# Kernel tuning notes

Measured on AMD Instinct MI355X. Metric: run time of the kernel, lower is better.

The kernel has to match this reference:

```python
import jax, jax.numpy as jnp
import numpy as np

NUM_HEADS = 16

def setup_inputs() -> dict:
    key = jax.random.key(0)
    k1, k2, k3 = jax.random.split(key, 3)
    D = 1024
    return {
        "hidden_states": jax.random.normal(k1, (2, 2048, D), dtype=jnp.float32),
        "c_attn_w": jax.random.normal(k2, (D, 3 * D), dtype=jnp.float32) * 0.02,
        "c_attn_b": jnp.zeros((3 * D,), dtype=jnp.float32),
        "c_proj_w": jax.random.normal(k3, (D, D), dtype=jnp.float32) * 0.02,
        "c_proj_b": jnp.zeros((D,), dtype=jnp.float32),
    }

def reference(hidden_states, c_attn_w, c_attn_b, c_proj_w, c_proj_b):
    B, S, D = hidden_states.shape
    H = NUM_HEADS
    hd = D // H
    # Conv1D: x @ W + b, then split into q, k, v
    qkv = hidden_states @ c_attn_w + c_attn_b  # [B, S, 3D]
    q, k, v = jnp.split(qkv, 3, axis=-1)
    q = q.reshape(B, S, H, hd).transpose(0, 2, 1, 3)  # [B, H, S, hd]
    k = k.reshape(B, S, H, hd).transpose(0, 2, 1, 3)
    v = v.reshape(B, S, H, hd).transpose(0, 2, 1, 3)
    # scaled QK^T
    scores = jnp.einsum("bhqd,bhkd->bhqk", q, k) / jnp.asarray(hd ** 0.5, q.dtype)
    # causal mask (tril), masked positions set to dtype min per original code
    causal = jnp.tril(jnp.ones((S, S), dtype=bool))
    mask_value = jnp.finfo(scores.dtype).min
    scores = jnp.where(causal[None, None], scores, mask_value)
    attn = jax.nn.softmax(scores, axis=-1)
    out = jnp.einsum("bhqk,bhkd->bhqd", attn, v)  # [B, H, S, hd]
    out = out.transpose(0, 2, 1, 3).reshape(B, S, D)
    out = out @ c_proj_w + c_proj_b
    return out
```

## Files before the change

kernel.cpp:

```cpp
#include <hip/hip_runtime.h>
#include <hip/hip_bf16.h>
#include <math.h>

#define B_ 2
#define S_ 2048
#define D_ 1024
#define H_ 16
#define HD 64
#define M_ (B_ * S_)
#define N_QKV (3 * D_)

typedef short short8 __attribute__((ext_vector_type(8)));
typedef float floatx4 __attribute__((ext_vector_type(4)));

static __device__ __forceinline__ unsigned short f2bf(float x) {
    __hip_bfloat16 h = __float2bfloat16(x);
    unsigned short u;
    __builtin_memcpy(&u, &h, sizeof(u));
    return u;
}
static __device__ __forceinline__ float bf2f(unsigned short b) {
    union { unsigned u; float f; } v; v.u = ((unsigned)b) << 16;
    return v.f;
}
static __device__ __forceinline__ void split2(float x, unsigned short& h, unsigned short& l) {
    h = f2bf(x);
    l = f2bf(x - bf2f(h));
}

static __device__ __forceinline__ void dma16(const void* g, void* l) {
    __builtin_amdgcn_global_load_lds(
        (const __attribute__((address_space(1))) unsigned int*)g,
        (__attribute__((address_space(3))) unsigned int*)l,
        16, 0, 0);
}

__global__ __launch_bounds__(256) void prep_wT(
    const float* __restrict__ W, int N,
    unsigned short* __restrict__ Thi, unsigned short* __restrict__ Tlo)
{
    __shared__ float Ws[64][68];
    const int t  = threadIdx.x;
    const int n0 = blockIdx.x * 64, k0 = blockIdx.y * 64;
    {
        const int kl = t >> 4, nl = (t & 15) * 4;
        const float* src = W + (size_t)(k0 + kl) * N + n0 + nl;
#pragma unroll
        for (int g = 0; g < 4; g++)
            *(float4*)&Ws[kl + g * 16][nl] = *(const float4*)(src + (size_t)g * 16 * N);
    }
    __syncthreads();
    {
        const int nl = t >> 2, ks = (t & 3) * 16;
        short8 h0, h1, l0, l1;
#pragma unroll
        for (int j = 0; j < 8; j++) {
            unsigned short hh, ll;
            split2(Ws[ks + j][nl], hh, ll);
            h0[j] = (short)hh; l0[j] = (short)ll;
        }
#pragma unroll
        for (int j = 0; j < 8; j++) {
            unsigned short hh, ll;
            split2(Ws[ks + 8 + j][nl], hh, ll);
            h1[j] = (short)hh; l1[j] = (short)ll;
        }
        unsigned short* dh = Thi + (size_t)(n0 + nl) * D_ + k0 + ks;
        unsigned short* dl = Tlo + (size_t)(n0 + nl) * D_ + k0 + ks;
        *(short8*)dh = h0; *(short8*)(dh + 8) = h1;
        *(short8*)dl = l0; *(short8*)(dl + 8) = l1;
    }
}

__global__ __launch_bounds__(256) void gemm_qkv(
    const float* __restrict__ A,
    const unsigned short* __restrict__ BThi, const unsigned short* __restrict__ BTlo,
    const float* __restrict__ bias,
    unsigned short* __restrict__ Qhi, unsigned short* __restrict__ Qlo,
    unsigned short* __restrict__ Khi, unsigned short* __restrict__ Klo,
    unsigned short* __restrict__ vThi, unsigned short* __restrict__ vTlo)
{
    __shared__ unsigned short sAh[128 * 32], sAl[128 * 32];
    __shared__ unsigned short sBh[128 * 32], sBl[128 * 32];

    const int t    = threadIdx.x;
    const int m0   = blockIdx.y * 128, n0 = blockIdx.x * 128;
    const int lane = t & 63, wave = t >> 6;
    const int lm   = lane & 15, quad = lane >> 4;
    const int wm   = (wave >> 1) * 64, wn = (wave & 1) * 64;

    const int srow = t >> 1, sseg = (t & 1) * 16;
    const float* Ap = A + (size_t)(m0 + srow) * D_ + sseg;

    const int lrow = lane >> 2, lcol = (lane & 3) * 8;
    const unsigned short* gBh0 = BThi + (size_t)(n0 + wave * 32 + lrow) * D_ + lcol;
    const unsigned short* gBl0 = BTlo + (size_t)(n0 + wave * 32 + lrow) * D_ + lcol;
    unsigned short* lBh0 = sBh + wave * 1024 + lane * 8;
    unsigned short* lBl0 = sBl + wave * 1024 + lane * 8;

    floatx4 acc[4][4];
#pragma unroll
    for (int i = 0; i < 4; i++)
#pragma unroll
        for (int j = 0; j < 4; j++)
#pragma unroll
            for (int r = 0; r < 4; r++) acc[i][j][r] = 0.f;

    float4 af[4];
    af[0] = *(const float4*)(Ap);     af[1] = *(const float4*)(Ap + 4);
    af[2] = *(const float4*)(Ap + 8); af[3] = *(const float4*)(Ap + 12);

    for (int k0 = 0; k0 < D_; k0 += 32) {
        short8 ah0, ah1, al0, al1;
#pragma unroll
        for (int g = 0; g < 4; g++) {
            float xs[4] = {af[g].x, af[g].y, af[g].z, af[g].w};
#pragma unroll
            for (int e = 0; e < 4; e++) {
                unsigned short hh, ll;
                split2(xs[e], hh, ll);
                if (g < 2) { ah0[g * 4 + e] = (short)hh; al0[g * 4 + e] = (short)ll; }
                else       { ah1[(g - 2) * 4 + e] = (short)hh; al1[(g - 2) * 4 + e] = (short)ll; }
            }
        }
        __syncthreads();
        {
            unsigned short* a = &sAh[srow * 32 + sseg];
            unsigned short* b = &sAl[srow * 32 + sseg];
            *(short8*)a = ah0; *(short8*)(a + 8) = ah1;
            *(short8*)b = al0; *(short8*)(b + 8) = al1;
        }
        dma16(gBh0 + k0, lBh0);
        dma16(gBh0 + (size_t)16 * D_ + k0, lBh0 + 512);
        dma16(gBl0 + k0, lBl0);
        dma16(gBl0 + (size_t)16 * D_ + k0, lBl0 + 512);
        __syncthreads();

        if (k0 + 32 < D_) {
            const float* an = Ap + k0 + 32;
            af[0] = *(const float4*)(an);     af[1] = *(const float4*)(an + 4);
            af[2] = *(const float4*)(an + 8); af[3] = *(const float4*)(an + 12);
        }

        short8 bhf[4], blf[4];
#pragma unroll
        for (int nb = 0; nb < 4; nb++) {
            const int r = wn + nb * 16 + lm;
            bhf[nb] = *(const short8*)&sBh[r * 32 + quad * 8];
            blf[nb] = *(const short8*)&sBl[r * 32 + quad * 8];
        }
#pragma unroll
        for (int mb = 0; mb < 4; mb++) {
            const int r = wm + mb * 16 + lm;
            short8 ah = *(const short8*)&sAh[r * 32 + quad * 8];
            short8 al = *(const short8*)&sAl[r * 32 + quad * 8];
#pragma unroll
            for (int nb = 0; nb < 4; nb++) {
                acc[mb][nb] = __builtin_amdgcn_mfma_f32_16x16x32_bf16(ah, bhf[nb], acc[mb][nb], 0, 0, 0);
                acc[mb][nb] = __builtin_amdgcn_mfma_f32_16x16x32_bf16(al, bhf[nb], acc[mb][nb], 0, 0, 0);
                acc[mb][nb] = __builtin_amdgcn_mfma_f32_16x16x32_bf16(ah, blf[nb], acc[mb][nb], 0, 0, 0);
            }
        }
    }

    const int nmode = n0 >> 10;
    if (nmode == 0) {
#pragma unroll
        for (int nb = 0; nb < 4; nb++) {
            const int c = n0 + wn + nb * 16 + lm;
            const float bv = bias[c];
#pragma unroll
            for (int mb = 0; mb < 4; mb++) {
                const int rowb = m0 + wm + mb * 16 + quad * 4;
#pragma unroll
                for (int r = 0; r < 4; r++) {
                    unsigned short hh, ll;
                    split2((acc[mb][nb][r] + bv) * 0.125f, hh, ll);
                    Qhi[(size_t)(rowb + r) * D_ + c] = hh;
                    Qlo[(size_t)(rowb + r) * D_ + c] = ll;
                }
            }
        }
    } else if (nmode == 1) {
#pragma unroll
        for (int nb = 0; nb < 4; nb++) {
            const int c = n0 + wn + nb * 16 + lm;
            const float bv = bias[c];
            const int cq = c - 1024;
#pragma unroll
            for (int mb = 0; mb < 4; mb++) {
                const int rowb = m0 + wm + mb * 16 + quad * 4;
#pragma unroll
                for (int r = 0; r < 4; r++) {
                    unsigned short hh, ll;
                    split2(acc[mb][nb][r] + bv, hh, ll);
                    Khi[(size_t)(rowb + r) * D_ + cq] = hh;
                    Klo[(size_t)(rowb + r) * D_ + cq] = ll;
                }
            }
        }
    } else {
#pragma unroll
        for (int nb = 0; nb < 4; nb++) {
            const int c = n0 + wn + nb * 16 + lm;
            const float bv = bias[c];
            const int cq = c - 2048;
            const int hh_ = cq >> 6, dd = cq & 63;
#pragma unroll
            for (int mb = 0; mb < 4; mb++) {
                const int rowb = m0 + wm + mb * 16 + quad * 4;
                const int bb = rowb >> 11, ss = rowb & 2047;
                unsigned short hv[4], lv[4];
#pragma unroll
                for (int r = 0; r < 4; r++)
                    split2(acc[mb][nb][r] + bv, hv[r], lv[r]);
                const size_t idx = ((size_t)((bb * 16 + hh_) * 64 + dd)) * S_ + ss;
                *(uint2*)&vThi[idx] = make_uint2((unsigned)hv[0] | ((unsigned)hv[1] << 16),
                                                 (unsigned)hv[2] | ((unsigned)hv[3] << 16));
                *(uint2*)&vTlo[idx] = make_uint2((unsigned)lv[0] | ((unsigned)lv[1] << 16),
                                                 (unsigned)lv[2] | ((unsigned)lv[3] << 16));
            }
        }
    }
}

__global__ __launch_bounds__(256) void gemm_out(
    const unsigned short* __restrict__ Ahi, const unsigned short* __restrict__ Alo,
    const unsigned short* __restrict__ BThi, const unsigned short* __restrict__ BTlo,
    const float* __restrict__ bias, float* __restrict__ C)
{
    __shared__ unsigned short sAh[128 * 32], sAl[128 * 32];
    __shared__ unsigned short sBh[128 * 32], sBl[128 * 32];

    const int t    = threadIdx.x;
    const int m0   = blockIdx.y * 128, n0 = blockIdx.x * 128;
    const int lane = t & 63, wave = t >> 6;
    const int lm   = lane & 15, quad = lane >> 4;
    const int wm   = (wave >> 1) * 64, wn = (wave & 1) * 64;

    const int lrow = lane >> 2, lcol = (lane & 3) * 8;
    const unsigned short* gAh = Ahi + (size_t)(m0 + wave * 32 + lrow) * D_ + lcol;
    const unsigned short* gAl = Alo + (size_t)(m0 + wave * 32 + lrow) * D_ + lcol;
    const unsigned short* gBh = BThi + (size_t)(n0 + wave * 32 + lrow) * D_ + lcol;
    const unsigned short* gBl = BTlo + (size_t)(n0 + wave * 32 + lrow) * D_ + lcol;
    unsigned short* lAh = sAh + wave * 1024 + lane * 8;
    unsigned short* lAl = sAl + wave * 1024 + lane * 8;
    unsigned short* lBh = sBh + wave * 1024 + lane * 8;
    unsigned short* lBl = sBl + wave * 1024 + lane * 8;

    floatx4 acc[4][4];
#pragma unroll
    for (int i = 0; i < 4; i++)
#pragma unroll
        for (int j = 0; j < 4; j++)
#pragma unroll
            for (int r = 0; r < 4; r++) acc[i][j][r] = 0.f;

    for (int k0 = 0; k0 < D_; k0 += 32) {
        __syncthreads();
        dma16(gAh + k0, lAh);
        dma16(gAh + (size_t)16 * D_ + k0, lAh + 512);
        dma16(gAl + k0, lAl);
        dma16(gAl + (size_t)16 * D_ + k0, lAl + 512);
        dma16(gBh + k0, lBh);
        dma16(gBh + (size_t)16 * D_ + k0, lBh + 512);
        dma16(gBl + k0, lBl);
        dma16(gBl + (size_t)16 * D_ + k0, lBl + 512);
        __syncthreads();

        short8 bhf[4], blf[4];
#pragma unroll
        for (int nb = 0; nb < 4; nb++) {
            const int r = wn + nb * 16 + lm;
            bhf[nb] = *(const short8*)&sBh[r * 32 + quad * 8];
            blf[nb] = *(const short8*)&sBl[r * 32 + quad * 8];
        }
#pragma unroll
        for (int mb = 0; mb < 4; mb++) {
            const int r = wm + mb * 16 + lm;
            short8 ah = *(const short8*)&sAh[r * 32 + quad * 8];
            short8 al = *(const short8*)&sAl[r * 32 + quad * 8];
#pragma unroll
            for (int nb = 0; nb < 4; nb++) {
                acc[mb][nb] = __builtin_amdgcn_mfma_f32_16x16x32_bf16(ah, bhf[nb], acc[mb][nb], 0, 0, 0);
                acc[mb][nb] = __builtin_amdgcn_mfma_f32_16x16x32_bf16(al, bhf[nb], acc[mb][nb], 0, 0, 0);
                acc[mb][nb] = __builtin_amdgcn_mfma_f32_16x16x32_bf16(ah, blf[nb], acc[mb][nb], 0, 0, 0);
            }
        }
    }

#pragma unroll
    for (int nb = 0; nb < 4; nb++) {
        const int c = n0 + wn + nb * 16 + lm;
        const float bv = bias[c];
#pragma unroll
        for (int mb = 0; mb < 4; mb++) {
            const int rowb = m0 + wm + mb * 16 + quad * 4;
#pragma unroll
            for (int r = 0; r < 4; r++)
                C[(size_t)(rowb + r) * D_ + c] = acc[mb][nb][r] + bv;
        }
    }
}

#define PST 72

__global__ __launch_bounds__(512, 4) void flash_attn_mfma(
    unsigned short* QAhi, unsigned short* QAlo,
    const unsigned short* __restrict__ Khi, const unsigned short* __restrict__ Klo,
    const unsigned short* __restrict__ vThi, const unsigned short* __restrict__ vTlo)
{
    __shared__ unsigned short KhiS[64 * PST];
    __shared__ unsigned short KloS[64 * PST];
    __shared__ unsigned short VhiS[64 * PST];
    __shared__ unsigned short VloS[64 * PST];
    __shared__ unsigned short PhS[128 * PST];
    __shared__ unsigned short PlS[128 * PST];

    const int t    = threadIdx.x;
    const int pj   = blockIdx.x;
    const int bh   = blockIdx.y;
    const int b    = bh >> 4, h = bh & 15;
    const int lane = t & 63, w = t >> 6;
    const int lm   = lane & 15, quad = lane >> 4;

    const int srow = t >> 3;
    const int sseg = (t & 7) * 8;

    const unsigned short* Kh_b = Khi + (size_t)(b * S_) * D_ + h * HD + sseg;
    const unsigned short* Kl_b = Klo + (size_t)(b * S_) * D_ + h * HD + sseg;
    const unsigned short* Vh_b = vThi + ((size_t)((b * 16 + h) * 64 + srow)) * S_ + sseg;
    const unsigned short* Vl_b = vTlo + ((size_t)((b * 16 + h) * 64 + srow)) * S_ + sseg;

    for (int phse = 0; phse < 2; phse++) {
        const int qt = phse ? (15 - pj) : pj;
        const int q0 = qt * 128;
        const int ntiles = 2 * qt + 2;
        const int wdiag = (q0 >> 6) + (w >> 2);

        short8 qh[2], ql[2];
        {
            const size_t qoff = (size_t)(b * S_ + q0 + 16 * w + lm) * D_ + h * HD + quad * 8;
            qh[0] = *(const short8*)&QAhi[qoff];
            qh[1] = *(const short8*)&QAhi[qoff + 32];
            ql[0] = *(const short8*)&QAlo[qoff];
            ql[1] = *(const short8*)&QAlo[qoff + 32];
        }

        float lsum[4] = {0.f, 0.f, 0.f, 0.f};
        floatx4 o[4];
#pragma unroll
        for (int nb = 0; nb < 4; nb++)
#pragma unroll
            for (int r = 0; r < 4; r++) o[nb][r] = 0.f;

        uint4 pkh, pkl, pvh, pvl;
        pkh = *(const uint4*)(Kh_b + (size_t)srow * D_);
        pkl = *(const uint4*)(Kl_b + (size_t)srow * D_);
        pvh = *(const uint4*)(Vh_b);
        pvl = *(const uint4*)(Vl_b);

        for (int kt = 0; kt < ntiles; kt++) {
            __syncthreads();
            *(uint4*)&KhiS[srow * PST + sseg] = pkh;
            *(uint4*)&KloS[srow * PST + sseg] = pkl;
            *(uint4*)&VhiS[srow * PST + sseg] = pvh;
            *(uint4*)&VloS[srow * PST + sseg] = pvl;
            __syncthreads();

            if (kt + 1 < ntiles) {
                const int k1 = (kt + 1) * 64;
                pkh = *(const uint4*)(Kh_b + (size_t)(k1 + srow) * D_);
                pkl = *(const uint4*)(Kl_b + (size_t)(k1 + srow) * D_);
                pvh = *(const uint4*)(Vh_b + k1);
                pvl = *(const uint4*)(Vl_b + k1);
            }

            if (kt <= wdiag) {
                floatx4 sa[4];
#pragma unroll
                for (int nb = 0; nb < 4; nb++)
#pragma unroll
                    for (int r = 0; r < 4; r++) sa[nb][r] = 0.f;
#pragma unroll
                for (int s = 0; s < 2; s++) {
#pragma unroll
                    for (int nb = 0; nb < 4; nb++) {
                        short8 kh = *(const short8*)&KhiS[(nb * 16 + lm) * PST + s * 32 + quad * 8];
                        short8 kl = *(const short8*)&KloS[(nb * 16 + lm) * PST + s * 32 + quad * 8];
                        sa[nb] = __builtin_amdgcn_mfma_f32_16x16x32_bf16(qh[s], kh, sa[nb], 0, 0, 0);
                        sa[nb] = __builtin_amdgcn_mfma_f32_16x16x32_bf16(ql[s], kh, sa[nb], 0, 0, 0);
                        sa[nb] = __builtin_amdgcn_mfma_f32_16x16x32_bf16(qh[s], kl, sa[nb], 0, 0, 0);
                    }
                }

                const bool diag = (kt == wdiag);
                const int kbase = kt * 64;
#pragma unroll
                for (int r = 0; r < 4; r++) {
                    const int qabs = q0 + 16 * w + 4 * quad + r;
                    const int rloc = 16 * w + 4 * quad + r;
#pragma unroll
                    for (int nb = 0; nb < 4; nb++) {
                        float p = __expf(sa[nb][r]);
                        if (diag && (kbase + 16 * nb + lm > qabs)) p = 0.f;
                        lsum[r] += p;
                        unsigned short hh, ll;
                        split2(p, hh, ll);
                        PhS[rloc * PST + 16 * nb + lm] = hh;
                        PlS[rloc * PST + 16 * nb + lm] = ll;
                    }
                }

#pragma unroll
                for (int ks = 0; ks < 2; ks++) {
                    short8 pf = *(const short8*)&PhS[(16 * w + lm) * PST + ks * 32 + quad * 8];
                    short8 pg = *(const short8*)&PlS[(16 * w + lm) * PST + ks * 32 + quad * 8];
#pragma unroll
                    for (int nb = 0; nb < 4; nb++) {
                        short8 vhf = *(const short8*)&VhiS[(16 * nb + lm) * PST + ks * 32 + quad * 8];
                        short8 vlf = *(const short8*)&VloS[(16 * nb + lm) * PST + ks * 32 + quad * 8];
                        o[nb] = __builtin_amdgcn_mfma_f32_16x16x32_bf16(pf, vhf, o[nb], 0, 0, 0);
                        o[nb] = __builtin_amdgcn_mfma_f32_16x16x32_bf16(pg, vhf, o[nb], 0, 0, 0);
                        o[nb] = __builtin_amdgcn_mfma_f32_16x16x32_bf16(pf, vlf, o[nb], 0, 0, 0);
                    }
                }
            }
        }

#pragma unroll
        for (int r = 0; r < 4; r++) {
            float l = lsum[r];
            l += __shfl_xor(l, 1);
            l += __shfl_xor(l, 2);
            l += __shfl_xor(l, 4);
            l += __shfl_xor(l, 8);
            const float inv = 1.f / l;
            const size_t rowoff =
                (size_t)(b * S_ + q0 + 16 * w + 4 * quad + r) * D_ + h * HD + lm;
#pragma unroll
            for (int nb = 0; nb < 4; nb++) {
                unsigned short hh, ll;
                split2(o[nb][r] * inv, hh, ll);
                QAhi[rowoff + 16 * nb] = hh;
                QAlo[rowoff + 16 * nb] = ll;
            }
        }
    }
}

extern "C" void kernel_launch(void* const* d_in, const int* in_sizes, int n_in,
                              void* d_out, int out_size, void* d_ws, size_t ws_size,
                              hipStream_t stream)
{
    const float* hs     = (const float*)d_in[0];
    const float* attn_w = (const float*)d_in[1];
    const float* attn_b = (const float*)d_in[2];
    const float* proj_w = (const float*)d_in[3];
    const float* proj_b = (const float*)d_in[4];
    float* outp = (float*)d_out;

    const size_t QE = (size_t)M_ * D_;
    const size_t WQ = (size_t)D_ * N_QKV;
    unsigned short* Qhi   = (unsigned short*)d_ws;
    unsigned short* Qlo   = Qhi + QE;
    unsigned short* Khi   = Qlo + QE;
    unsigned short* Klo   = Khi + QE;
    unsigned short* vThi  = Klo + QE;
    unsigned short* vTlo  = vThi + QE;
    unsigned short* WqThi = vTlo + QE;
    unsigned short* WqTlo = WqThi + WQ;
    unsigned short* WpThi = WqTlo + WQ;
    unsigned short* WpTlo = WpThi + (size_t)D_ * D_;

    dim3 blk(256);
    prep_wT<<<dim3(N_QKV / 64, D_ / 64), blk, 0, stream>>>(attn_w, N_QKV, WqThi, WqTlo);
    prep_wT<<<dim3(D_ / 64, D_ / 64), blk, 0, stream>>>(proj_w, D_, WpThi, WpTlo);
    gemm_qkv<<<dim3(N_QKV / 128, M_ / 128), blk, 0, stream>>>(
        hs, WqThi, WqTlo, attn_b, Qhi, Qlo, Khi, Klo, vThi, vTlo);
    flash_attn_mfma<<<dim3(8, B_ * H_), dim3(512), 0, stream>>>(
        Qhi, Qlo, Khi, Klo, vThi, vTlo);
    gemm_out<<<dim3(D_ / 128, M_ / 128), blk, 0, stream>>>(
        Qhi, Qlo, WpThi, WpTlo, proj_b, outp);
}
```

Measured before the change: 315.7 us.

## Double-buffer LDS in GEMMs and attention, retile and swizzle output GEMM

Adds two-stage LDS double buffering to the QKV GEMM, the output GEMM and the flash-attention K/V tiles. Each tile's load is issued before the current tile's MFMAs, so only one barrier per iteration is needed. The output GEMM moves to 128x64 tiles on a 1D grid with an L2-friendly swizzle, giving 512 blocks for better CU coverage. Attention wraps its MFMA phases in s_setprio and relaxes launch_bounds occupancy from 4 to 2. The extra LDS and registers may reduce occupancy.

```diff
diff --git a/kernel.cpp b/kernel.cpp
--- a/kernel.cpp
+++ b/kernel.cpp
@@ -80,8 +80,8 @@
     unsigned short* __restrict__ Khi, unsigned short* __restrict__ Klo,
     unsigned short* __restrict__ vThi, unsigned short* __restrict__ vTlo)
 {
-    __shared__ unsigned short sAh[128 * 32], sAl[128 * 32];
-    __shared__ unsigned short sBh[128 * 32], sBl[128 * 32];
+    __shared__ unsigned short sAh[2][128 * 32], sAl[2][128 * 32];
+    __shared__ unsigned short sBh[2][128 * 32], sBl[2][128 * 32];
 
     const int t    = threadIdx.x;
     const int m0   = blockIdx.y * 128, n0 = blockIdx.x * 128;
@@ -95,8 +95,7 @@
     const int lrow = lane >> 2, lcol = (lane & 3) * 8;
     const unsigned short* gBh0 = BThi + (size_t)(n0 + wave * 32 + lrow) * D_ + lcol;
     const unsigned short* gBl0 = BTlo + (size_t)(n0 + wave * 32 + lrow) * D_ + lcol;
-    unsigned short* lBh0 = sBh + wave * 1024 + lane * 8;
-    unsigned short* lBl0 = sBl + wave * 1024 + lane * 8;
+    const int ldst = wave * 1024 + lane * 8;
 
     floatx4 acc[4][4];
 #pragma unroll
@@ -110,50 +109,66 @@
     af[0] = *(const float4*)(Ap);     af[1] = *(const float4*)(Ap + 4);
     af[2] = *(const float4*)(Ap + 8); af[3] = *(const float4*)(Ap + 12);
 
+#define CVT_WRITE_A(BUF)                                                        \
+    {                                                                           \
+        short8 ah0, ah1, al0, al1;                                              \
+        float xs0[8] = {af[0].x, af[0].y, af[0].z, af[0].w,                     \
+                        af[1].x, af[1].y, af[1].z, af[1].w};                    \
+        float xs1[8] = {af[2].x, af[2].y, af[2].z, af[2].w,                     \
+                        af[3].x, af[3].y, af[3].z, af[3].w};                    \
+        _Pragma("unroll")                                                       \
+        for (int e = 0; e < 8; e++) {                                           \
+            unsigned short hh, ll;                                              \
+            split2(xs0[e], hh, ll); ah0[e] = (short)hh; al0[e] = (short)ll;     \
+            split2(xs1[e], hh, ll); ah1[e] = (short)hh; al1[e] = (short)ll;     \
+        }                                                                       \
+        unsigned short* a_ = &sAh[BUF][srow * 32 + sseg];                       \
+        unsigned short* b_ = &sAl[BUF][srow * 32 + sseg];                       \
+        *(short8*)a_ = ah0; *(short8*)(a_ + 8) = ah1;                           \
+        *(short8*)b_ = al0; *(short8*)(b_ + 8) = al1;                           \
+    }
+
+#define DMA_B(BUF, K0)                                                          \
+    {                                                                           \
+        dma16(gBh0 + (K0), &sBh[BUF][ldst]);                                    \
+        dma16(gBh0 + (size_t)16 * D_ + (K0), &sBh[BUF][ldst + 512]);            \
+        dma16(gBl0 + (K0), &sBl[BUF][ldst]);                                    \
+        dma16(gBl0 + (size_t)16 * D_ + (K0), &sBl[BUF][ldst + 512]);            \
+    }
+
+    CVT_WRITE_A(0);
+    DMA_B(0, 0);
+    {
+        const float* an = Ap + 32;
+        af[0] = *(const float4*)(an);     af[1] = *(const float4*)(an + 4);
+        af[2] = *(const float4*)(an + 8); af[3] = *(const float4*)(an + 12);
+    }
+    __syncthreads();
+
+    int cur = 0;
     for (int k0 = 0; k0 < D_; k0 += 32) {
-        short8 ah0, ah1, al0, al1;
-#pragma unroll
-        for (int g = 0; g < 4; g++) {
-            float xs[4] = {af[g].x, af[g].y, af[g].z, af[g].w};
-#pragma unroll
-            for (int e = 0; e < 4; e++) {
-                unsigned short hh, ll;
-                split2(xs[e], hh, ll);
-                if (g < 2) { ah0[g * 4 + e] = (short)hh; al0[g * 4 + e] = (short)ll; }
-                else       { ah1[(g - 2) * 4 + e] = (short)hh; al1[(g - 2) * 4 + e] = (short)ll; }
-            }
-        }
-        __syncthreads();
-        {
-            unsigned short* a = &sAh[srow * 32 + sseg];
-            unsigned short* b = &sAl[srow * 32 + sseg];
-            *(short8*)a = ah0; *(short8*)(a + 8) = ah1;
-            *(short8*)b = al0; *(short8*)(b + 8) = al1;
-        }
-        dma16(gBh0 + k0, lBh0);
-        dma16(gBh0 + (size_t)16 * D_ + k0, lBh0 + 512);
-        dma16(gBl0 + k0, lBl0);
-        dma16(gBl0 + (size_t)16 * D_ + k0, lBl0 + 512);
-        __syncthreads();
-
         if (k0 + 32 < D_) {
-            const float* an = Ap + k0 + 32;
-            af[0] = *(const float4*)(an);     af[1] = *(const float4*)(an + 4);
-            af[2] = *(const float4*)(an + 8); af[3] = *(const float4*)(an + 12);
+            DMA_B(cur ^ 1, k0 + 32);
+            CVT_WRITE_A(cur ^ 1);
+            if (k0 + 64 < D_) {
+                const float* an = Ap + k0 + 64;
+                af[0] = *(const float4*)(an);     af[1] = *(const float4*)(an + 4);
+                af[2] = *(const float4*)(an + 8); af[3] = *(const float4*)(an + 12);
+            }
         }
 
         short8 bhf[4], blf[4];
 #pragma unroll
         for (int nb = 0; nb < 4; nb++) {
             const int r = wn + nb * 16 + lm;
-            bhf[nb] = *(const short8*)&sBh[r * 32 + quad * 8];
-            blf[nb] = *(const short8*)&sBl[r * 32 + quad * 8];
+            bhf[nb] = *(const short8*)&sBh[cur][r * 32 + quad * 8];
+            blf[nb] = *(const short8*)&sBl[cur][r * 32 + quad * 8];
         }
 #pragma unroll
         for (int mb = 0; mb < 4; mb++) {
             const int r = wm + mb * 16 + lm;
-            short8 ah = *(const short8*)&sAh[r * 32 + quad * 8];
-            short8 al = *(const short8*)&sAl[r * 32 + quad * 8];
+            short8 ah = *(const short8*)&sAh[cur][r * 32 + quad * 8];
+            short8 al = *(const short8*)&sAl[cur][r * 32 + quad * 8];
 #pragma unroll
             for (int nb = 0; nb < 4; nb++) {
                 acc[mb][nb] = __builtin_amdgcn_mfma_f32_16x16x32_bf16(ah, bhf[nb], acc[mb][nb], 0, 0, 0);
@@ -161,7 +176,11 @@
                 acc[mb][nb] = __builtin_amdgcn_mfma_f32_16x16x32_bf16(ah, blf[nb], acc[mb][nb], 0, 0, 0);
             }
         }
-    }
+        __syncthreads();
+        cur ^= 1;
+    }
+#undef CVT_WRITE_A
+#undef DMA_B
 
     const int nmode = n0 >> 10;
     if (nmode == 0) {
@@ -229,91 +248,100 @@
     const unsigned short* __restrict__ BThi, const unsigned short* __restrict__ BTlo,
     const float* __restrict__ bias, float* __restrict__ C)
 {
-    __shared__ unsigned short sAh[128 * 32], sAl[128 * 32];
-    __shared__ unsigned short sBh[128 * 32], sBl[128 * 32];
-
-    const int t    = threadIdx.x;
-    const int m0   = blockIdx.y * 128, n0 = blockIdx.x * 128;
+    __shared__ unsigned short sAh[2][128 * 32], sAl[2][128 * 32];
+    __shared__ unsigned short sBh[2][64 * 32],  sBl[2][64 * 32];
+
+    const int t   = threadIdx.x;
+    const int lid = blockIdx.x;
+    const int swz = (lid & 7) * 64 + (lid >> 3);
+    const int bx  = swz & 15, by = swz >> 4;
+    const int m0  = by * 128, n0 = bx * 64;
     const int lane = t & 63, wave = t >> 6;
     const int lm   = lane & 15, quad = lane >> 4;
-    const int wm   = (wave >> 1) * 64, wn = (wave & 1) * 64;
+    const int wm   = (wave >> 1) * 64, wn = (wave & 1) * 32;
 
     const int lrow = lane >> 2, lcol = (lane & 3) * 8;
     const unsigned short* gAh = Ahi + (size_t)(m0 + wave * 32 + lrow) * D_ + lcol;
     const unsigned short* gAl = Alo + (size_t)(m0 + wave * 32 + lrow) * D_ + lcol;
-    const unsigned short* gBh = BThi + (size_t)(n0 + wave * 32 + lrow) * D_ + lcol;
-    const unsigned short* gBl = BTlo + (size_t)(n0 + wave * 32 + lrow) * D_ + lcol;
-    unsigned short* lAh = sAh + wave * 1024 + lane * 8;
-    unsigned short* lAl = sAl + wave * 1024 + lane * 8;
-    unsigned short* lBh = sBh + wave * 1024 + lane * 8;
-    unsigned short* lBl = sBl + wave * 1024 + lane * 8;
-
-    floatx4 acc[4][4];
+    const unsigned short* gBh = BThi + (size_t)(n0 + (t >> 2)) * D_ + (t & 3) * 8;
+    const unsigned short* gBl = BTlo + (size_t)(n0 + (t >> 2)) * D_ + (t & 3) * 8;
+    const int adst = wave * 1024 + lane * 8;
+    const int bdst = t * 8;
+
+#define STAGE_OUT(BUF, K0)                                                      \
+    {                                                                           \
+        dma16(gAh + (K0), &sAh[BUF][adst]);                                     \
+        dma16(gAh + (size_t)16 * D_ + (K0), &sAh[BUF][adst + 512]);             \
+        dma16(gAl + (K0), &sAl[BUF][adst]);                                     \
+        dma16(gAl + (size_t)16 * D_ + (K0), &sAl[BUF][adst + 512]);             \
+        dma16(gBh + (K0), &sBh[BUF][bdst]);                                     \
+        dma16(gBl + (K0), &sBl[BUF][bdst]);                                     \
+    }
+
+    floatx4 acc[4][2];
 #pragma unroll
     for (int i = 0; i < 4; i++)
 #pragma unroll
-        for (int j = 0; j < 4; j++)
+        for (int j = 0; j < 2; j++)
 #pragma unroll
             for (int r = 0; r < 4; r++) acc[i][j][r] = 0.f;
 
+    STAGE_OUT(0, 0);
+    __syncthreads();
+
+    int cur = 0;
     for (int k0 = 0; k0 < D_; k0 += 32) {
-        __syncthreads();
-        dma16(gAh + k0, lAh);
-        dma16(gAh + (size_t)16 * D_ + k0, lAh + 512);
-        dma16(gAl + k0, lAl);
-        dma16(gAl + (size_t)16 * D_ + k0, lAl + 512);
-        dma16(gBh + k0, lBh);
-        dma16(gBh + (size_t)16 * D_ + k0, lBh + 512);
-        dma16(gBl + k0, lBl);
-        dma16(gBl + (size_t)16 * D_ + k0, lBl + 512);
-        __syncthreads();
-
-        short8 bhf[4], blf[4];
-#pragma unroll
-        for (int nb = 0; nb < 4; nb++) {
+        if (k0 + 32 < D_) STAGE_OUT(cur ^ 1, k0 + 32);
+
+        short8 bhf[2], blf[2];
+#pragma unroll
+        for (int nb = 0; nb < 2; nb++) {
             const int r = wn + nb * 16 + lm;
-            bhf[nb] = *(const short8*)&sBh[r * 32 + quad * 8];
-            blf[nb] = *(const short8*)&sBl[r * 32 + quad * 8];
+            bhf[nb] = *(const short8*)&sBh[cur][r * 32 + quad * 8];
+            blf[nb] = *(const short8*)&sBl[cur][r * 32 + quad * 8];
         }
 #pragma unroll
         for (int mb = 0; mb < 4; mb++) {
             const int r = wm + mb * 16 + lm;
-            short8 ah = *(const short8*)&sAh[r * 32 + quad * 8];
-            short8 al = *(const short8*)&sAl[r * 32 + quad * 8];
-#pragma unroll
-            for (int nb = 0; nb < 4; nb++) {
+            short8 ah = *(const short8*)&sAh[cur][r * 32 + quad * 8];
+            short8 al = *(const short8*)&sAl[cur][r * 32 + quad * 8];
+#pragma unroll
+            for (int nb = 0; nb < 2; nb++) {
                 acc[mb][nb] = __builtin_amdgcn_mfma_f32_16x16x32_bf16(ah, bhf[nb], acc[mb][nb], 0, 0, 0);
                 acc[mb][nb] = __builtin_amdgcn_mfma_f32_16x16x32_bf16(al, bhf[nb], acc[mb][nb], 0, 0, 0);
                 acc[mb][nb] = __builtin_amdgcn_mfma_f32_16x16x32_bf16(ah, blf[nb], acc[mb][nb], 0, 0, 0);
             }
         }
-    }
-
-#pragma unroll
-    for (int nb = 0; nb < 4; nb++) {
-        const int c = n0 + wn + nb * 16 + lm;
-        const float bv = bias[c];
+        __syncthreads();
+        cur ^= 1;
+    }
+#undef STAGE_OUT
+
+#pragma unroll
+    for (int nb = 0; nb < 2; nb++) {
+        const int col = n0 + wn + nb * 16 + lm;
+        const float bv = bias[col];
 #pragma unroll
         for (int mb = 0; mb < 4; mb++) {
             const int rowb = m0 + wm + mb * 16 + quad * 4;
 #pragma unroll
             for (int r = 0; r < 4; r++)
-                C[(size_t)(rowb + r) * D_ + c] = acc[mb][nb][r] + bv;
+                C[(size_t)(rowb + r) * D_ + col] = acc[mb][nb][r] + bv;
         }
     }
 }
 
 #define PST 72
 
-__global__ __launch_bounds__(512, 4) void flash_attn_mfma(
+__global__ __launch_bounds__(512, 2) void flash_attn_mfma(
     unsigned short* QAhi, unsigned short* QAlo,
     const unsigned short* __restrict__ Khi, const unsigned short* __restrict__ Klo,
     const unsigned short* __restrict__ vThi, const unsigned short* __restrict__ vTlo)
 {
-    __shared__ unsigned short KhiS[64 * PST];
-    __shared__ unsigned short KloS[64 * PST];
-    __shared__ unsigned short VhiS[64 * PST];
-    __shared__ unsigned short VloS[64 * PST];
+    __shared__ unsigned short KhS[2][64 * PST];
+    __shared__ unsigned short KlS[2][64 * PST];
+    __shared__ unsigned short VhS[2][64 * PST];
+    __shared__ unsigned short VlS[2][64 * PST];
     __shared__ unsigned short PhS[128 * PST];
     __shared__ unsigned short PlS[128 * PST];
 
@@ -331,6 +359,8 @@
     const unsigned short* Kl_b = Klo + (size_t)(b * S_) * D_ + h * HD + sseg;
     const unsigned short* Vh_b = vThi + ((size_t)((b * 16 + h) * 64 + srow)) * S_ + sseg;
     const unsigned short* Vl_b = vTlo + ((size_t)((b * 16 + h) * 64 + srow)) * S_ + sseg;
+
+    const int sdst = srow * PST + sseg;
 
     for (int phse = 0; phse < 2; phse++) {
         const int qt = phse ? (15 - pj) : pj;
@@ -359,17 +389,28 @@
         pkl = *(const uint4*)(Kl_b + (size_t)srow * D_);
         pvh = *(const uint4*)(Vh_b);
         pvl = *(const uint4*)(Vl_b);
-
+        *(uint4*)&KhS[0][sdst] = pkh;
+        *(uint4*)&KlS[0][sdst] = pkl;
+        *(uint4*)&VhS[0][sdst] = pvh;
+        *(uint4*)&VlS[0][sdst] = pvl;
+        if (ntiles > 1) {
+            pkh = *(const uint4*)(Kh_b + (size_t)(64 + srow) * D_);
+            pkl = *(const uint4*)(Kl_b + (size_t)(64 + srow) * D_);
+            pvh = *(const uint4*)(Vh_b + 64);
+            pvl = *(const uint4*)(Vl_b + 64);
+        }
+        __syncthreads();
+
+        int cur = 0;
         for (int kt = 0; kt < ntiles; kt++) {
-            __syncthreads();
-            *(uint4*)&KhiS[srow * PST + sseg] = pkh;
-            *(uint4*)&KloS[srow * PST + sseg] = pkl;
-            *(uint4*)&VhiS[srow * PST + sseg] = pvh;
-            *(uint4*)&VloS[srow * PST + sseg] = pvl;
-            __syncthreads();
-
             if (kt + 1 < ntiles) {
-                const int k1 = (kt + 1) * 64;
+                *(uint4*)&KhS[cur ^ 1][sdst] = pkh;
+                *(uint4*)&KlS[cur ^ 1][sdst] = pkl;
+                *(uint4*)&VhS[cur ^ 1][sdst] = pvh;
+                *(uint4*)&VlS[cur ^ 1][sdst] = pvl;
+            }
+            if (kt + 2 < ntiles) {
+                const int k1 = (kt + 2) * 64;
                 pkh = *(const uint4*)(Kh_b + (size_t)(k1 + srow) * D_);
                 pkl = *(const uint4*)(Kl_b + (size_t)(k1 + srow) * D_);
                 pvh = *(const uint4*)(Vh_b + k1);
@@ -382,17 +423,19 @@
                 for (int nb = 0; nb < 4; nb++)
 #pragma unroll
                     for (int r = 0; r < 4; r++) sa[nb][r] = 0.f;
+                __builtin_amdgcn_s_setprio(1);
 #pragma unroll
                 for (int s = 0; s < 2; s++) {
 #pragma unroll
                     for (int nb = 0; nb < 4; nb++) {
-                        short8 kh = *(const short8*)&KhiS[(nb * 16 + lm) * PST + s * 32 + quad * 8];
-                        short8 kl = *(const short8*)&KloS[(nb * 16 + lm) * PST + s * 32 + quad * 8];
+                        short8 kh = *(const short8*)&KhS[cur][(nb * 16 + lm) * PST + s * 32 + quad * 8];
+                        short8 kl = *(const short8*)&KlS[cur][(nb * 16 + lm) * PST + s * 32 + quad * 8];
                         sa[nb] = __builtin_amdgcn_mfma_f32_16x16x32_bf16(qh[s], kh, sa[nb], 0, 0, 0);
                         sa[nb] = __builtin_amdgcn_mfma_f32_16x16x32_bf16(ql[s], kh, sa[nb], 0, 0, 0);
                         sa[nb] = __builtin_amdgcn_mfma_f32_16x16x32_bf16(qh[s], kl, sa[nb], 0, 0, 0);
                     }
                 }
+                __builtin_amdgcn_s_setprio(0);
 
                 const bool diag = (kt == wdiag);
                 const int kbase = kt * 64;
@@ -412,20 +455,24 @@
                     }
                 }
 
+                __builtin_amdgcn_s_setprio(1);
 #pragma unroll
                 for (int ks = 0; ks < 2; ks++) {
                     short8 pf = *(const short8*)&PhS[(16 * w + lm) * PST + ks * 32 + quad * 8];
                     short8 pg = *(const short8*)&PlS[(16 * w + lm) * PST + ks * 32 + quad * 8];
 #pragma unroll
                     for (int nb = 0; nb < 4; nb++) {
-                        short8 vhf = *(const short8*)&VhiS[(16 * nb + lm) * PST + ks * 32 + quad * 8];
-                        short8 vlf = *(const short8*)&VloS[(16 * nb + lm) * PST + ks * 32 + quad * 8];
+                        short8 vhf = *(const short8*)&VhS[cur][(16 * nb + lm) * PST + ks * 32 + quad * 8];
+                        short8 vlf = *(const short8*)&VlS[cur][(16 * nb + lm) * PST + ks * 32 + quad * 8];
                         o[nb] = __builtin_amdgcn_mfma_f32_16x16x32_bf16(pf, vhf, o[nb], 0, 0, 0);
                         o[nb] = __builtin_amdgcn_mfma_f32_16x16x32_bf16(pg, vhf, o[nb], 0, 0, 0);
                         o[nb] = __builtin_amdgcn_mfma_f32_16x16x32_bf16(pf, vlf, o[nb], 0, 0, 0);
                     }
                 }
-            }
+                __builtin_amdgcn_s_setprio(0);
+            }
+            __syncthreads();
+            cur ^= 1;
         }
 
 #pragma unroll
@@ -480,6 +527,6 @@
         hs, WqThi, WqTlo, attn_b, Qhi, Qlo, Khi, Klo, vThi, vTlo);
     flash_attn_mfma<<<dim3(8, B_ * H_), dim3(512), 0, stream>>>(
         Qhi, Qlo, Khi, Klo, vThi, vTlo);
-    gemm_out<<<dim3(D_ / 128, M_ / 128), blk, 0, stream>>>(
+    gemm_out<<<dim3(512), blk, 0, stream>>>(
         Qhi, Qlo, WpThi, WpTlo, proj_b, outp);
 }
```

New measurement: 319.9 us. No clear change (+1.3%).
